# Kernel tuning notes

Measured on AMD Instinct MI355X. Metric: run time of the kernel, lower is better.

Reference implementation:

```python
import jax, jax.numpy as jnp
import numpy as np

B, P, K = 32, 1024, 16  # clouds, points per cloud, neighbors


def setup_inputs() -> dict:
    key = jax.random.key(0)
    ks = jax.random.split(key, 5)
    N, C, H, D = B * P, 64, 128, 3
    x = jax.random.normal(ks[0], (N, C), dtype=jnp.float32)
    pos = jax.random.normal(ks[1], (N, D), dtype=jnp.float32)
    batch = jnp.arange(N, dtype=jnp.int64) // P  # cloud id per node
    W_e = jax.random.normal(ks[2], (2 * C, H), dtype=jnp.float32) * 0.05
    b_e = jnp.zeros((H,), dtype=jnp.float32)
    W_sc = jax.random.normal(ks[3], (C, H), dtype=jnp.float32) * 0.05
    b_sc = jnp.zeros((H,), dtype=jnp.float32)
    return {"x": x, "pos": pos, "batch": batch,
            "W_e": W_e, "b_e": b_e, "W_sc": W_sc, "b_sc": b_sc}


def _knn_idx(posb):
    # posb: [B, P, D] -> idx [B, P, K]: K nearest neighbors (sources) per target node,
    # within each cloud, excluding self (loop=False in torch_geometric.knn_graph).
    sq = jnp.sum(posb * posb, axis=-1)                       # [B, P]
    d2 = sq[:, :, None] + sq[:, None, :] - 2.0 * jnp.einsum('bid,bjd->bij', posb, posb)
    d2 = d2 + jnp.eye(P, dtype=posb.dtype)[None] * jnp.finfo(posb.dtype).max / 2
    _, idx = jax.lax.top_k(-d2, K)                           # [B, P, K]
    return idx


def reference(x, pos, batch, W_e, b_e, W_sc, b_sc):
    C = x.shape[-1]
    xb = x.reshape(B, P, C)
    posb = pos.reshape(B, P, -1)
    idx = _knn_idx(posb)                                     # [B, P, K]
    # gather neighbor (source) features per target node
    x_j = jax.vmap(lambda xc, ic: xc[ic])(xb, idx)           # [B, P, K, C]
    x_i = xb[:, :, None, :]                                  # [B, P, 1, C]
    # EdgeConv message: nn([x_i, x_j - x_i]), here Linear + ReLU
    e = jnp.concatenate([jnp.broadcast_to(x_i, x_j.shape), x_j - x_i], axis=-1)  # [B,P,K,2C]
    msg = jax.nn.relu(jnp.einsum('bpke,eh->bpkh', e, W_e) + b_e)
    agg = jnp.max(msg, axis=2)                               # max aggregation -> [B, P, H]
    shortcut = x @ W_sc + b_sc                               # [N, H]
    out = agg.reshape(-1, agg.shape[-1]) + shortcut
    return out
```

## Files before the change

kernel.cpp:

```cpp
#include <hip/hip_runtime.h>
#include <float.h>
#include <stdint.h>

#define BATCHES 32
#define P 1024
#define KNN 16
#define C 64
#define H 128
#define N (BATCHES * P)
#define NCOLS 384
#define SPLITS 8
#define CPS 128
#define PADH 132

typedef short short8 __attribute__((ext_vector_type(8)));
typedef float floatx4 __attribute__((ext_vector_type(4)));

__device__ __forceinline__ unsigned short f2bf(float f) {
    unsigned u = __float_as_uint(f);
    unsigned r = (u + 0x7FFF + ((u >> 16) & 1)) >> 16;
    return (unsigned short)r;
}

__global__ __launch_bounds__(256) void prep_w(
    const float* __restrict__ W_e, const float* __restrict__ b_e,
    const float* __restrict__ W_sc, const float* __restrict__ b_sc,
    unsigned short* __restrict__ WT, float* __restrict__ bias)
{
    int i = blockIdx.x * 256 + threadIdx.x;
    int col = i >> 6, c = i & 63;
    float w;
    if (col < 128)      w = W_e[c * 128 + col] - W_e[(64 + c) * 128 + col];
    else if (col < 256) w = W_e[(64 + c) * 128 + (col - 128)];
    else                w = W_sc[c * 128 + (col - 256)];
    WT[col * 64 + c] = f2bf(w);
    if (c == 0) {
        bias[col] = (col < 128) ? b_e[col] : (col < 256 ? 0.0f : b_sc[col - 256]);
    }
}

struct alignas(16) F4 { float x, y, z, w; };

struct PA {
    F4    spos[P + 8];
    float lists[SPLITS][16][64];
    unsigned short offs[SPLITS][64];
    unsigned short cnts[SPLITS][64];
    float Tq[64];
};
struct PB {
    unsigned short Ubuf[64][PADH];
    unsigned short Vbuf[64][PADH];
    unsigned short Sbuf[64][PADH];
};

__global__ __launch_bounds__(512) void knn_gemm_kernel(
    const float* __restrict__ pos, const float* __restrict__ X,
    const unsigned short* __restrict__ WT, const float* __restrict__ bias,
    int* __restrict__ idx_out,
    unsigned short* __restrict__ U, unsigned short* __restrict__ V,
    unsigned short* __restrict__ S)
{
    __shared__ __align__(16) char smraw[sizeof(PA)];
    PA* A  = (PA*)smraw;
    PB* Bm = (PB*)smraw;

    int t = threadIdx.x;
    int q = t & 63, s = t >> 6;
    int blk = blockIdx.x;
    int batch = blk >> 4;
    int qblk  = blk & 15;
    int iloc  = qblk * 64 + q;

    const float* pb = pos + (size_t)batch * P * 3;
    for (int j = t; j < P; j += 512) {
        float x = pb[j * 3 + 0], y = pb[j * 3 + 1], z = pb[j * 3 + 2];
        float sq = __fadd_rn(__fadd_rn(__fmul_rn(x, x), __fmul_rn(y, y)),
                             __fmul_rn(z, z));
        A->spos[j] = F4{x, y, z, sq};
    }
    __syncthreads();

    F4 me = A->spos[iloc];
    const int j0 = s * CPS;

    float d[16];
#pragma unroll
    for (int k = 0; k < 16; ++k) d[k] = FLT_MAX;

    auto dist = [&](const F4& c, int j) -> float {
        float dot = __fadd_rn(__fadd_rn(__fmul_rn(me.x, c.x), __fmul_rn(me.y, c.y)),
                              __fmul_rn(me.z, c.z));
        float d2 = __fadd_rn(__fadd_rn(me.w, c.w), __fmul_rn(-2.0f, dot));
        return (j == iloc) ? FLT_MAX : d2;
    };
    auto insert = [&](float d2) {
#pragma unroll
        for (int k = 15; k >= 1; --k)
            d[k] = __builtin_amdgcn_fmed3f(d[k - 1], d2, d[k]);
        d[0] = fminf(d[0], d2);
    };

    {
        F4 c0 = A->spos[j0 + 0], c1 = A->spos[j0 + 1];
        F4 c2 = A->spos[j0 + 2], c3 = A->spos[j0 + 3];
#pragma unroll 2
        for (int jj = 0; jj < CPS; jj += 4) {
            F4 n0 = A->spos[j0 + jj + 4];
            F4 n1 = A->spos[j0 + jj + 5];
            F4 n2 = A->spos[j0 + jj + 6];
            F4 n3 = A->spos[j0 + jj + 7];
            insert(dist(c0, j0 + jj + 0));
            insert(dist(c1, j0 + jj + 1));
            insert(dist(c2, j0 + jj + 2));
            insert(dist(c3, j0 + jj + 3));
            c0 = n0; c1 = n1; c2 = n2; c3 = n3;
        }
    }
#pragma unroll
    for (int k = 0; k < 16; ++k) A->lists[s][k][q] = d[k];
    __syncthreads();

    if (s == 0) {
        float v0 = A->lists[0][0][q], v1 = A->lists[1][0][q];
        float v2 = A->lists[2][0][q], v3 = A->lists[3][0][q];
        float v4 = A->lists[4][0][q], v5 = A->lists[5][0][q];
        float v6 = A->lists[6][0][q], v7 = A->lists[7][0][q];
        float w0 = A->lists[0][1][q], w1 = A->lists[1][1][q];
        float w2 = A->lists[2][1][q], w3 = A->lists[3][1][q];
        float w4 = A->lists[4][1][q], w5 = A->lists[5][1][q];
        float w6 = A->lists[6][1][q], w7 = A->lists[7][1][q];
        int n0 = 0, n1 = 0, n2 = 0, n3 = 0, n4 = 0, n5 = 0, n6 = 0, n7 = 0;
        float T = 0.0f;
#pragma unroll 1
        for (int k = 0; k < 16; ++k) {
            float mn = fminf(fminf(fminf(v0, v1), fminf(v2, v3)),
                             fminf(fminf(v4, v5), fminf(v6, v7)));
            if      (v0 == mn) { n0++; v0 = w0; w0 = (n0 + 1 < 16) ? A->lists[0][n0 + 1][q] : FLT_MAX; }
            else if (v1 == mn) { n1++; v1 = w1; w1 = (n1 + 1 < 16) ? A->lists[1][n1 + 1][q] : FLT_MAX; }
            else if (v2 == mn) { n2++; v2 = w2; w2 = (n2 + 1 < 16) ? A->lists[2][n2 + 1][q] : FLT_MAX; }
            else if (v3 == mn) { n3++; v3 = w3; w3 = (n3 + 1 < 16) ? A->lists[3][n3 + 1][q] : FLT_MAX; }
            else if (v4 == mn) { n4++; v4 = w4; w4 = (n4 + 1 < 16) ? A->lists[4][n4 + 1][q] : FLT_MAX; }
            else if (v5 == mn) { n5++; v5 = w5; w5 = (n5 + 1 < 16) ? A->lists[5][n5 + 1][q] : FLT_MAX; }
            else if (v6 == mn) { n6++; v6 = w6; w6 = (n6 + 1 < 16) ? A->lists[6][n6 + 1][q] : FLT_MAX; }
            else               { n7++; v7 = w7; w7 = (n7 + 1 < 16) ? A->lists[7][n7 + 1][q] : FLT_MAX; }
            T = mn;
        }
        A->Tq[q] = T;
        int off = 0;
        A->offs[0][q] = (unsigned short)off; A->cnts[0][q] = (unsigned short)n0; off += n0;
        A->offs[1][q] = (unsigned short)off; A->cnts[1][q] = (unsigned short)n1; off += n1;
        A->offs[2][q] = (unsigned short)off; A->cnts[2][q] = (unsigned short)n2; off += n2;
        A->offs[3][q] = (unsigned short)off; A->cnts[3][q] = (unsigned short)n3; off += n3;
        A->offs[4][q] = (unsigned short)off; A->cnts[4][q] = (unsigned short)n4; off += n4;
        A->offs[5][q] = (unsigned short)off; A->cnts[5][q] = (unsigned short)n5; off += n5;
        A->offs[6][q] = (unsigned short)off; A->cnts[6][q] = (unsigned short)n6; off += n6;
        A->offs[7][q] = (unsigned short)off; A->cnts[7][q] = (unsigned short)n7;
    }
    __syncthreads();

    {
        float T  = A->Tq[q];
        int   cap = A->cnts[s][q];
        int   gb  = ((blk << 6) + q) * KNN + A->offs[s][q];
        int   base = batch * P;
        int   cnt = 0;

        F4 c0 = A->spos[j0 + 0], c1 = A->spos[j0 + 1];
        F4 c2 = A->spos[j0 + 2], c3 = A->spos[j0 + 3];
#pragma unroll 2
        for (int jj = 0; jj < CPS; jj += 4) {
            F4 n0 = A->spos[j0 + jj + 4];
            F4 n1 = A->spos[j0 + jj + 5];
            F4 n2 = A->spos[j0 + jj + 6];
            F4 n3 = A->spos[j0 + jj + 7];
#pragma unroll
            for (int u = 0; u < 4; ++u) {
                const F4& c = (u == 0) ? c0 : (u == 1) ? c1 : (u == 2) ? c2 : c3;
                int j = j0 + jj + u;
                float d2 = dist(c, j);
                if (d2 <= T && cnt < cap) {
                    idx_out[gb + cnt] = base + j;
                    cnt++;
                }
            }
            c0 = n0; c1 = n1; c2 = n2; c3 = n3;
        }
    }
    __syncthreads();

    {
        int mt = s & 3, nh = s >> 2;
        int m0 = blk * 64 + mt * 16;
        int lm = q & 15, kg = q >> 4;

        const float4* arow = (const float4*)(X + (size_t)(m0 + lm) * 64 + kg * 8);
        float4 f0 = arow[0], f1 = arow[1];
        float4 f2 = arow[8], f3 = arow[9];
        short8 a0, a1;
        a0[0] = (short)f2bf(f0.x); a0[1] = (short)f2bf(f0.y);
        a0[2] = (short)f2bf(f0.z); a0[3] = (short)f2bf(f0.w);
        a0[4] = (short)f2bf(f1.x); a0[5] = (short)f2bf(f1.y);
        a0[6] = (short)f2bf(f1.z); a0[7] = (short)f2bf(f1.w);
        a1[0] = (short)f2bf(f2.x); a1[1] = (short)f2bf(f2.y);
        a1[2] = (short)f2bf(f2.z); a1[3] = (short)f2bf(f2.w);
        a1[4] = (short)f2bf(f3.x); a1[5] = (short)f2bf(f3.y);
        a1[6] = (short)f2bf(f3.z); a1[7] = (short)f2bf(f3.w);

#pragma unroll 4
        for (int nt = nh * 12; nt < nh * 12 + 12; ++nt) {
            const short8* brow = (const short8*)(WT + (size_t)(nt * 16 + lm) * 64 + kg * 8);
            short8 b0 = brow[0];
            short8 b1 = brow[4];
            floatx4 acc = {0.0f, 0.0f, 0.0f, 0.0f};
            acc = __builtin_amdgcn_mfma_f32_16x16x32_bf16(a0, b0, acc, 0, 0, 0);
            acc = __builtin_amdgcn_mfma_f32_16x16x32_bf16(a1, b1, acc, 0, 0, 0);

            int col = nt * 16 + lm;
            float bv = bias[col];
#pragma unroll
            for (int r = 0; r < 4; ++r) {
                int row = mt * 16 + kg * 4 + r;
                unsigned short val = f2bf(acc[r] + bv);
                if (col < 128)      Bm->Ubuf[row][col] = val;
                else if (col < 256) Bm->Vbuf[row][col - 128] = val;
                else                Bm->Sbuf[row][col - 256] = val;
            }
        }
    }
    __syncthreads();

    {
        uint2* Ug = (uint2*)U + (size_t)blk * 2048;
        uint2* Vg = (uint2*)V + (size_t)blk * 2048;
        uint2* Sg = (uint2*)S + (size_t)blk * 2048;
#pragma unroll
        for (int i = t; i < 2048; i += 512) {
            int row = i >> 5, off = (i & 31) * 4;
            Ug[i] = *(const uint2*)&Bm->Ubuf[row][off];
            Vg[i] = *(const uint2*)&Bm->Vbuf[row][off];
            Sg[i] = *(const uint2*)&Bm->Sbuf[row][off];
        }
    }
}

__global__ __launch_bounds__(256) void final_kernel(
    const int* __restrict__ idx, const unsigned short* __restrict__ U,
    const unsigned short* __restrict__ V, const unsigned short* __restrict__ S,
    float* __restrict__ out)
{
    int t = threadIdx.x;
    __shared__ int nbr[16][KNN];
    ((int*)nbr)[t] = idx[(size_t)blockIdx.x * 256 + t];
    __syncthreads();

    int pl = t >> 4;
    int c8 = t & 15;
    size_t p = (size_t)blockIdx.x * 16 + pl;

    uint4 uu = ((const uint4*)(U + p * H))[c8];
    uint4 ss = ((const uint4*)(S + p * H))[c8];

    float m0 = -FLT_MAX, m1 = -FLT_MAX, m2 = -FLT_MAX, m3 = -FLT_MAX;
    float m4 = -FLT_MAX, m5 = -FLT_MAX, m6 = -FLT_MAX, m7 = -FLT_MAX;
#pragma unroll
    for (int k = 0; k < KNN; ++k) {
        int row = nbr[pl][k];
        uint4 vv = *(const uint4*)(V + (size_t)row * H + c8 * 8);
        m0 = fmaxf(m0, __uint_as_float(vv.x << 16));
        m1 = fmaxf(m1, __uint_as_float(vv.x & 0xFFFF0000u));
        m2 = fmaxf(m2, __uint_as_float(vv.y << 16));
        m3 = fmaxf(m3, __uint_as_float(vv.y & 0xFFFF0000u));
        m4 = fmaxf(m4, __uint_as_float(vv.z << 16));
        m5 = fmaxf(m5, __uint_as_float(vv.z & 0xFFFF0000u));
        m6 = fmaxf(m6, __uint_as_float(vv.w << 16));
        m7 = fmaxf(m7, __uint_as_float(vv.w & 0xFFFF0000u));
    }

    float4 oa, ob;
    oa.x = fmaxf(__uint_as_float(uu.x << 16)         + m0, 0.0f) + __uint_as_float(ss.x << 16);
    oa.y = fmaxf(__uint_as_float(uu.x & 0xFFFF0000u) + m1, 0.0f) + __uint_as_float(ss.x & 0xFFFF0000u);
    oa.z = fmaxf(__uint_as_float(uu.y << 16)         + m2, 0.0f) + __uint_as_float(ss.y << 16);
    oa.w = fmaxf(__uint_as_float(uu.y & 0xFFFF0000u) + m3, 0.0f) + __uint_as_float(ss.y & 0xFFFF0000u);
    ob.x = fmaxf(__uint_as_float(uu.z << 16)         + m4, 0.0f) + __uint_as_float(ss.z << 16);
    ob.y = fmaxf(__uint_as_float(uu.z & 0xFFFF0000u) + m5, 0.0f) + __uint_as_float(ss.z & 0xFFFF0000u);
    ob.z = fmaxf(__uint_as_float(uu.w << 16)         + m6, 0.0f) + __uint_as_float(ss.w << 16);
    ob.w = fmaxf(__uint_as_float(uu.w & 0xFFFF0000u) + m7, 0.0f) + __uint_as_float(ss.w & 0xFFFF0000u);
    ((float4*)(out + p * H))[c8 * 2]     = oa;
    ((float4*)(out + p * H))[c8 * 2 + 1] = ob;
}

extern "C" void kernel_launch(void* const* d_in, const int* in_sizes, int n_in,
                              void* d_out, int out_size, void* d_ws, size_t ws_size,
                              hipStream_t stream)
{
    const float* x    = (const float*)d_in[0];
    const float* pos  = (const float*)d_in[1];
    const float* W_e  = (const float*)d_in[3];
    const float* b_e  = (const float*)d_in[4];
    const float* W_sc = (const float*)d_in[5];
    const float* b_sc = (const float*)d_in[6];
    float* out = (float*)d_out;

    char* ws = (char*)d_ws;
    const size_t OFF_IDX  = 0;
    const size_t OFF_U    = 2ull << 20;
    const size_t OFF_V    = OFF_U + (8ull << 20);
    const size_t OFF_S    = OFF_V + (8ull << 20);
    const size_t OFF_WT   = OFF_S + (8ull << 20);
    const size_t OFF_BIAS = OFF_WT + 49152;

    int*            idx  = (int*)(ws + OFF_IDX);
    unsigned short* U    = (unsigned short*)(ws + OFF_U);
    unsigned short* V    = (unsigned short*)(ws + OFF_V);
    unsigned short* S    = (unsigned short*)(ws + OFF_S);
    unsigned short* WT   = (unsigned short*)(ws + OFF_WT);
    float*          bias = (float*)(ws + OFF_BIAS);

    prep_w<<<(NCOLS * C) / 256, 256, 0, stream>>>(W_e, b_e, W_sc, b_sc, WT, bias);
    knn_gemm_kernel<<<512, 512, 0, stream>>>(pos, x, WT, bias, idx, U, V, S);
    final_kernel<<<N / 16, 256, 0, stream>>>(idx, U, V, S, out);
}
```

Measured before the change: 146.2 us.

## Halve queries per block to 32 and make the top-k merge branchless

The fused kNN+GEMM kernel now handles 32 query points per block with 256 threads instead of 64 with 512. That doubles the grid to 1024 blocks and allows up to 4 resident blocks per CU via launch bounds. The MFMA tiling is remapped to 4 waves covering 2 row tiles by 2 column halves, and the output copy is resized to match. The 8-way sorted-list merge is rewritten as a branchless unrolled select over arrays, avoiding divergent if-chains at the cost of more LDS reads per step. Each block still stages the full cloud's 1024 positions, so that load work is doubled overall.

```diff
diff --git a/kernel.cpp b/kernel.cpp
--- a/kernel.cpp
+++ b/kernel.cpp
@@ -11,6 +11,7 @@
 #define NCOLS 384
 #define SPLITS 8
 #define CPS 128
+#define QB 32
 #define PADH 132
 
 typedef short short8 __attribute__((ext_vector_type(8)));
@@ -43,18 +44,18 @@
 
 struct PA {
     F4    spos[P + 8];
-    float lists[SPLITS][16][64];
-    unsigned short offs[SPLITS][64];
-    unsigned short cnts[SPLITS][64];
-    float Tq[64];
+    float lists[SPLITS][16][QB];
+    unsigned short offs[SPLITS][QB];
+    unsigned short cnts[SPLITS][QB];
+    float Tq[QB];
 };
 struct PB {
-    unsigned short Ubuf[64][PADH];
-    unsigned short Vbuf[64][PADH];
-    unsigned short Sbuf[64][PADH];
+    unsigned short Ubuf[QB][PADH];
+    unsigned short Vbuf[QB][PADH];
+    unsigned short Sbuf[QB][PADH];
 };
 
-__global__ __launch_bounds__(512) void knn_gemm_kernel(
+__global__ __launch_bounds__(256, 4) void knn_gemm_kernel(
     const float* __restrict__ pos, const float* __restrict__ X,
     const unsigned short* __restrict__ WT, const float* __restrict__ bias,
     int* __restrict__ idx_out,
@@ -66,14 +67,14 @@
     PB* Bm = (PB*)smraw;
 
     int t = threadIdx.x;
-    int q = t & 63, s = t >> 6;
+    int q = t & 31, s = t >> 5;
     int blk = blockIdx.x;
-    int batch = blk >> 4;
-    int qblk  = blk & 15;
-    int iloc  = qblk * 64 + q;
+    int batch = blk >> 5;
+    int qblk  = blk & 31;
+    int iloc  = qblk * QB + q;
 
     const float* pb = pos + (size_t)batch * P * 3;
-    for (int j = t; j < P; j += 512) {
+    for (int j = t; j < P; j += 256) {
         float x = pb[j * 3 + 0], y = pb[j * 3 + 1], z = pb[j * 3 + 2];
         float sq = __fadd_rn(__fadd_rn(__fmul_rn(x, x), __fmul_rn(y, y)),
                              __fmul_rn(z, z));
@@ -122,47 +123,49 @@
     __syncthreads();
 
     if (s == 0) {
-        float v0 = A->lists[0][0][q], v1 = A->lists[1][0][q];
-        float v2 = A->lists[2][0][q], v3 = A->lists[3][0][q];
-        float v4 = A->lists[4][0][q], v5 = A->lists[5][0][q];
-        float v6 = A->lists[6][0][q], v7 = A->lists[7][0][q];
-        float w0 = A->lists[0][1][q], w1 = A->lists[1][1][q];
-        float w2 = A->lists[2][1][q], w3 = A->lists[3][1][q];
-        float w4 = A->lists[4][1][q], w5 = A->lists[5][1][q];
-        float w6 = A->lists[6][1][q], w7 = A->lists[7][1][q];
-        int n0 = 0, n1 = 0, n2 = 0, n3 = 0, n4 = 0, n5 = 0, n6 = 0, n7 = 0;
+        float v[8], wv[8];
+        int   n[8];
+#pragma unroll
+        for (int l = 0; l < 8; ++l) {
+            v[l]  = A->lists[l][0][q];
+            wv[l] = A->lists[l][1][q];
+            n[l]  = 0;
+        }
         float T = 0.0f;
 #pragma unroll 1
         for (int k = 0; k < 16; ++k) {
-            float mn = fminf(fminf(fminf(v0, v1), fminf(v2, v3)),
-                             fminf(fminf(v4, v5), fminf(v6, v7)));
-            if      (v0 == mn) { n0++; v0 = w0; w0 = (n0 + 1 < 16) ? A->lists[0][n0 + 1][q] : FLT_MAX; }
-            else if (v1 == mn) { n1++; v1 = w1; w1 = (n1 + 1 < 16) ? A->lists[1][n1 + 1][q] : FLT_MAX; }
-            else if (v2 == mn) { n2++; v2 = w2; w2 = (n2 + 1 < 16) ? A->lists[2][n2 + 1][q] : FLT_MAX; }
-            else if (v3 == mn) { n3++; v3 = w3; w3 = (n3 + 1 < 16) ? A->lists[3][n3 + 1][q] : FLT_MAX; }
-            else if (v4 == mn) { n4++; v4 = w4; w4 = (n4 + 1 < 16) ? A->lists[4][n4 + 1][q] : FLT_MAX; }
-            else if (v5 == mn) { n5++; v5 = w5; w5 = (n5 + 1 < 16) ? A->lists[5][n5 + 1][q] : FLT_MAX; }
-            else if (v6 == mn) { n6++; v6 = w6; w6 = (n6 + 1 < 16) ? A->lists[6][n6 + 1][q] : FLT_MAX; }
-            else               { n7++; v7 = w7; w7 = (n7 + 1 < 16) ? A->lists[7][n7 + 1][q] : FLT_MAX; }
+            float mn = fminf(fminf(fminf(v[0], v[1]), fminf(v[2], v[3])),
+                             fminf(fminf(v[4], v[5]), fminf(v[6], v[7])));
+            bool taken = false;
+#pragma unroll
+            for (int l = 0; l < 8; ++l) {
+                bool tk = (!taken) && (v[l] == mn);
+                taken = taken || tk;
+                int ni = n[l] + (tk ? 1 : 0);
+                int ri = ni + 1;
+                float rv = A->lists[l][(ri < 16) ? ri : 15][q];
+                float wnew = (ri < 16) ? rv : FLT_MAX;
+                v[l]  = tk ? wv[l] : v[l];
+                wv[l] = tk ? wnew  : wv[l];
+                n[l]  = ni;
+            }
             T = mn;
         }
         A->Tq[q] = T;
         int off = 0;
-        A->offs[0][q] = (unsigned short)off; A->cnts[0][q] = (unsigned short)n0; off += n0;
-        A->offs[1][q] = (unsigned short)off; A->cnts[1][q] = (unsigned short)n1; off += n1;
-        A->offs[2][q] = (unsigned short)off; A->cnts[2][q] = (unsigned short)n2; off += n2;
-        A->offs[3][q] = (unsigned short)off; A->cnts[3][q] = (unsigned short)n3; off += n3;
-        A->offs[4][q] = (unsigned short)off; A->cnts[4][q] = (unsigned short)n4; off += n4;
-        A->offs[5][q] = (unsigned short)off; A->cnts[5][q] = (unsigned short)n5; off += n5;
-        A->offs[6][q] = (unsigned short)off; A->cnts[6][q] = (unsigned short)n6; off += n6;
-        A->offs[7][q] = (unsigned short)off; A->cnts[7][q] = (unsigned short)n7;
+#pragma unroll
+        for (int l = 0; l < 8; ++l) {
+            A->offs[l][q] = (unsigned short)off;
+            A->cnts[l][q] = (unsigned short)n[l];
+            off += n[l];
+        }
     }
     __syncthreads();
 
     {
         float T  = A->Tq[q];
         int   cap = A->cnts[s][q];
-        int   gb  = ((blk << 6) + q) * KNN + A->offs[s][q];
+        int   gb  = (blk * QB + q) * KNN + A->offs[s][q];
         int   base = batch * P;
         int   cnt = 0;
 
@@ -190,9 +193,11 @@
     __syncthreads();
 
     {
-        int mt = s & 3, nh = s >> 2;
-        int m0 = blk * 64 + mt * 16;
-        int lm = q & 15, kg = q >> 4;
+        int w  = t >> 6;
+        int ln = t & 63;
+        int mt = w & 1, nh = w >> 1;
+        int m0 = blk * QB + mt * 16;
+        int lm = ln & 15, kg = ln >> 4;
 
         const float4* arow = (const float4*)(X + (size_t)(m0 + lm) * 64 + kg * 8);
         float4 f0 = arow[0], f1 = arow[1];
@@ -231,11 +236,11 @@
     __syncthreads();
 
     {
-        uint2* Ug = (uint2*)U + (size_t)blk * 2048;
-        uint2* Vg = (uint2*)V + (size_t)blk * 2048;
-        uint2* Sg = (uint2*)S + (size_t)blk * 2048;
-#pragma unroll
-        for (int i = t; i < 2048; i += 512) {
+        uint2* Ug = (uint2*)U + (size_t)blk * 1024;
+        uint2* Vg = (uint2*)V + (size_t)blk * 1024;
+        uint2* Sg = (uint2*)S + (size_t)blk * 1024;
+#pragma unroll
+        for (int i = t; i < 1024; i += 256) {
             int row = i >> 5, off = (i & 31) * 4;
             Ug[i] = *(const uint2*)&Bm->Ubuf[row][off];
             Vg[i] = *(const uint2*)&Bm->Vbuf[row][off];
@@ -318,6 +323,6 @@
     float*          bias = (float*)(ws + OFF_BIAS);
 
     prep_w<<<(NCOLS * C) / 256, 256, 0, stream>>>(W_e, b_e, W_sc, b_sc, WT, bias);
-    knn_gemm_kernel<<<512, 512, 0, stream>>>(pos, x, WT, bias, idx, U, V, S);
+    knn_gemm_kernel<<<N / QB, 256, 0, stream>>>(pos, x, WT, bias, idx, U, V, S);
     final_kernel<<<N / 16, 256, 0, stream>>>(idx, U, V, S, out);
 }
```

Result: faster. 142.4 us (-2.6%).
